# Optimization experiments

Measured on AMD Instinct MI355X. Metric: run time of the kernel, lower is better.

The kernel has to match this reference:

```python
import jax, jax.numpy as jnp
import numpy as np

EPS = 1e-08


def setup_inputs() -> dict:
    key = jax.random.key(0)
    k1, k2 = jax.random.split(key)
    z = jax.random.normal(k1, (32, 768, 32, 32), dtype=jnp.float32)
    memory = jax.random.normal(k2, (512, 768), dtype=jnp.float32)
    return {"z": z, "memory": memory}


def _l2_normalize(x, axis=-1, eps=1e-12):
    # Matches torch F.normalize(dim=-1): x / max(||x||, eps)
    n = jnp.sqrt(jnp.sum(x * x, axis=axis, keepdims=True))
    return x / jnp.maximum(n, eps)


def reference(z, memory):
    B, C, H, W = z.shape
    M = memory.shape[0]
    # (B, C, H, W) -> (B, H*W, C)
    z_flat = jnp.transpose(z, (0, 2, 3, 1)).reshape(B, H * W, C)
    z_norm = _l2_normalize(z_flat)
    mem_norm = _l2_normalize(memory)
    # cosine-similarity scores: (B, N, M)
    scores = jnp.einsum('bnc,mc->bnm', z_norm, mem_norm)
    w = jax.nn.softmax(scores, axis=-1)
    lam = 1.0 / M
    # hard-shrink sparsification: relu(w - lam) * w / (|w - lam| + eps)
    d = w - lam
    attn_w = jax.nn.relu(d) * w / (jnp.abs(d) + EPS)
    attn_w = attn_w / (jnp.sum(attn_w, axis=-1, keepdims=True) + EPS)
    # weighted readout against the RAW (un-normalized) memory
    z_hat_flat = jnp.einsum('bnm,mc->bnc', attn_w, memory)
    z_hat = jnp.transpose(z_hat_flat.reshape(B, H, W, C), (0, 3, 1, 2))
    return (z_hat, attn_w)
```

## Files before the change

### kernel.cpp

```cpp
#include <hip/hip_runtime.h>
#include <hip/hip_bf16.h>
#include <math.h>

typedef short short8 __attribute__((ext_vector_type(8)));
typedef float f32x4 __attribute__((ext_vector_type(4)));
typedef _Float16 f16x8 __attribute__((ext_vector_type(8)));

#define CC 768
#define NN 1024
#define RR 32768
#define MM 512
#define ZSTRIDE 786432
#define OUT_ATTN_OFF 25165824
#define SPLIT_SC 2048.0f
#define INV_SC   (1.0f / 2048.0f)

static __device__ __forceinline__ short f2bf(float f) {
    __hip_bfloat16 h = __float2bfloat16(f);
    return *reinterpret_cast<short*>(&h);
}

static __device__ __forceinline__ double fast_exp_neg(double x) {
    const double LOG2E = 1.4426950408889634074;
    const double LN2   = 0.6931471805599453094;
    const double MAGIC = 6755399441055744.0;
    double t = x * LOG2E;
    double c = t + MAGIC;
    double n = c - MAGIC;
    int ni = (int)__double2loint(c);
    double g = (t - n) * LN2;
    double r = 2.505210838544172e-08;
    r = fma(r, g, 2.755731922398589e-07);
    r = fma(r, g, 2.7557319223985893e-06);
    r = fma(r, g, 2.48015873015873e-05);
    r = fma(r, g, 1.984126984126984e-04);
    r = fma(r, g, 1.388888888888889e-03);
    r = fma(r, g, 8.333333333333333e-03);
    r = fma(r, g, 4.1666666666666664e-02);
    r = fma(r, g, 1.6666666666666666e-01);
    r = fma(r, g, 0.5);
    r = fma(r, g, 1.0);
    r = fma(r, g, 1.0);
    double sc = __hiloint2double((1023 + ni) << 20, 0);
    return r * sc;
}

static __device__ __forceinline__ double fast_rcp(double x) {
    double r = (double)(1.0f / (float)x);
    r = r * (2.0 - x * r);
    r = r * (2.0 - x * r);
    return r;
}

__global__ __launch_bounds__(256) void prep_mem_kernel(const float* __restrict__ memory,
                                                       _Float16* __restrict__ mem_h,
                                                       _Float16* __restrict__ mem_L,
                                                       short* __restrict__ memT_bf) {
    int m = blockIdx.x;
    int t = threadIdx.x;
    double ss = 0.0;
    for (int c = t; c < CC; c += 256) {
        float v = memory[m * CC + c];
        ss += (double)v * (double)v;
    }
    #pragma unroll
    for (int off = 32; off > 0; off >>= 1) ss += __shfl_xor(ss, off);
    __shared__ double red[4];
    __shared__ double invs;
    if ((t & 63) == 0) red[t >> 6] = ss;
    __syncthreads();
    if (t == 0) {
        double tot = red[0] + red[1] + red[2] + red[3];
        invs = 1.0 / fmax(sqrt(tot), 1e-12);
    }
    __syncthreads();
    float inv = (float)invs;
    for (int c = t; c < CC; c += 256) {
        float v  = memory[m * CC + c];
        float nv = v * inv;
        _Float16 h = (_Float16)nv;
        float r1 = nv - (float)h;
        mem_h[m * CC + c] = h;
        mem_L[m * CC + c] = (_Float16)(r1 * SPLIT_SC);
        memT_bf[c * MM + m] = f2bf(v);
    }
}

#define SWZ(row_, k_) ((((row_) << 5) + (k_)) ^ (((row_) & 7) << 3))
__global__ __launch_bounds__(256, 2) void scores_gemm_kernel(const float* __restrict__ z,
                                                             const _Float16* __restrict__ mem_h,
                                                             const _Float16* __restrict__ mem_L,
                                                             float* __restrict__ out_scores,
                                                             double* __restrict__ zinv_ws) {
    __shared__ _Float16 AT[2][2][4096];
    __shared__ _Float16 BT[2][2][4096];
    __shared__ double ssred[256];

    const int t    = threadIdx.x;
    const int lane = t & 63;
    const int wv   = t >> 6;
    const int lrow = lane & 15;
    const int gk   = lane >> 4;
    const int wr   = wv >> 1, wc = wv & 1;
    const int d = blockIdx.x;
    const int colblk = (d >> 3) & 3;
    const int rowblk = (d & 7) | ((d >> 5) << 3);
    const int row0 = rowblk * 128;
    const int b    = row0 >> 10;
    const int n0   = row0 & 1023;
    const int cB0  = colblk * 128;

    const int an   = t & 127;
    const int ak16 = (t >> 7) * 16;
    const float* zA = z + (size_t)b * ZSTRIDE + n0 + an;
    const int bc = t >> 1;
    const int kc = (t & 1) * 16;
    const _Float16* mhB = mem_h + (size_t)(cB0 + bc) * CC + kc;
    const _Float16* mLB = mem_L + (size_t)(cB0 + bc) * CC + kc;

    double ss = 0.0;
    f32x4 am[4][4], ax[4][4];
    #pragma unroll
    for (int fc = 0; fc < 4; ++fc)
        #pragma unroll
        for (int fn = 0; fn < 4; ++fn) {
            am[fc][fn] = (f32x4){0.f, 0.f, 0.f, 0.f};
            ax[fc][fn] = (f32x4){0.f, 0.f, 0.f, 0.f};
        }

    #define LOADS(kt_, av_, bh_, bl_)                                          \
        do {                                                                   \
            _Pragma("unroll")                                                  \
            for (int j = 0; j < 16; ++j)                                       \
                av_[j] = zA[(size_t)((kt_) * 32 + ak16 + j) * NN];             \
            bh_[0] = *reinterpret_cast<const f16x8*>(mhB + (kt_) * 32);        \
            bh_[1] = *reinterpret_cast<const f16x8*>(mhB + (kt_) * 32 + 8);    \
            bl_[0] = *reinterpret_cast<const f16x8*>(mLB + (kt_) * 32);        \
            bl_[1] = *reinterpret_cast<const f16x8*>(mLB + (kt_) * 32 + 8);    \
        } while (0)

    #define WRITES(bb_, av_, bh_, bl_)                                         \
        do {                                                                   \
            f16x8 h8a, l8a, h8b, l8b;                                          \
            _Pragma("unroll")                                                  \
            for (int j = 0; j < 8; ++j) {                                      \
                float v = av_[j];                                              \
                ss = fma((double)v, (double)v, ss);                            \
                _Float16 h = (_Float16)v;                                      \
                h8a[j] = h;                                                    \
                l8a[j] = (_Float16)((v - (float)h) * SPLIT_SC);                \
            }                                                                  \
            _Pragma("unroll")                                                  \
            for (int j = 0; j < 8; ++j) {                                      \
                float v = av_[8 + j];                                          \
                ss = fma((double)v, (double)v, ss);                            \
                _Float16 h = (_Float16)v;                                      \
                h8b[j] = h;                                                    \
                l8b[j] = (_Float16)((v - (float)h) * SPLIT_SC);                \
            }                                                                  \
            *reinterpret_cast<f16x8*>(&AT[bb_][0][SWZ(an, ak16)])     = h8a;   \
            *reinterpret_cast<f16x8*>(&AT[bb_][0][SWZ(an, ak16 + 8)]) = h8b;   \
            *reinterpret_cast<f16x8*>(&AT[bb_][1][SWZ(an, ak16)])     = l8a;   \
            *reinterpret_cast<f16x8*>(&AT[bb_][1][SWZ(an, ak16 + 8)]) = l8b;   \
            *reinterpret_cast<f16x8*>(&BT[bb_][0][SWZ(bc, kc)])       = bh_[0];\
            *reinterpret_cast<f16x8*>(&BT[bb_][0][SWZ(bc, kc + 8)])   = bh_[1];\
            *reinterpret_cast<f16x8*>(&BT[bb_][1][SWZ(bc, kc)])       = bl_[0];\
            *reinterpret_cast<f16x8*>(&BT[bb_][1][SWZ(bc, kc + 8)])   = bl_[1];\
        } while (0)

    {
        float av[16]; f16x8 bh8[2], bl8[2];
        LOADS(0, av, bh8, bl8);
        WRITES(0, av, bh8, bl8);
    }
    __syncthreads();

    #pragma unroll 1
    for (int kt = 0; kt < 24; ++kt) {
        const int cur = kt & 1;
        float av[16]; f16x8 bh8[2], bl8[2];
        if (kt < 23) LOADS(kt + 1, av, bh8, bl8);

        f16x8 ah[4], aL[4];
        #pragma unroll
        for (int fc = 0; fc < 4; ++fc) {
            ah[fc] = *reinterpret_cast<const f16x8*>(&AT[cur][0][SWZ(wr * 64 + fc * 16 + lrow, gk * 8)]);
            aL[fc] = *reinterpret_cast<const f16x8*>(&AT[cur][1][SWZ(wr * 64 + fc * 16 + lrow, gk * 8)]);
        }
        f16x8 bh[4], bL[4];
        #pragma unroll
        for (int fn = 0; fn < 4; ++fn) {
            bh[fn] = *reinterpret_cast<const f16x8*>(&BT[cur][0][SWZ(wc * 64 + fn * 16 + lrow, gk * 8)]);
            bL[fn] = *reinterpret_cast<const f16x8*>(&BT[cur][1][SWZ(wc * 64 + fn * 16 + lrow, gk * 8)]);
        }
        #pragma unroll
        for (int fn = 0; fn < 4; ++fn)
            #pragma unroll
            for (int fc = 0; fc < 4; ++fc) {
                am[fc][fn] = __builtin_amdgcn_mfma_f32_16x16x32_f16(ah[fc], bh[fn], am[fc][fn], 0, 0, 0);
                ax[fc][fn] = __builtin_amdgcn_mfma_f32_16x16x32_f16(aL[fc], bh[fn], ax[fc][fn], 0, 0, 0);
                ax[fc][fn] = __builtin_amdgcn_mfma_f32_16x16x32_f16(ah[fc], bL[fn], ax[fc][fn], 0, 0, 0);
            }

        if (kt < 23) WRITES(cur ^ 1, av, bh8, bl8);
        __syncthreads();
    }
    #undef LOADS
    #undef WRITES

    #pragma unroll
    for (int fc = 0; fc < 4; ++fc)
        #pragma unroll
        for (int fn = 0; fn < 4; ++fn)
            #pragma unroll
            for (int rg = 0; rg < 4; ++rg) {
                int row = row0 + wr * 64 + fc * 16 + gk * 4 + rg;
                int col = cB0 + wc * 64 + fn * 16 + lrow;
                out_scores[(size_t)row * MM + col] = am[fc][fn][rg] + ax[fc][fn][rg] * INV_SC;
            }

    ssred[t] = ss;
    __syncthreads();
    if (colblk == 0 && t < 128) {
        double tot = ssred[t] + ssred[t + 128];
        zinv_ws[row0 + t] = 1.0 / fmax(sqrt(tot), 1e-12);
    }
}
#undef SWZ

__global__ __launch_bounds__(256) void epilogue_kernel(float* __restrict__ attn,
                                                       const double* __restrict__ zinv_ws) {
    const int t    = threadIdx.x;
    const int lane = t & 63;
    const int wv   = t >> 6;
    const int row0 = blockIdx.x * 64;

    #pragma unroll 1
    for (int i = 0; i < 16; ++i) {
        int row = row0 + wv * 16 + i;
        double zi = zinv_ws[row];
        float* rp = attn + (size_t)row * MM;
        f32x4 x0 = *reinterpret_cast<const f32x4*>(&rp[lane * 4]);
        f32x4 x1 = *reinterpret_cast<const f32x4*>(&rp[256 + lane * 4]);
        double s0 = (double)x0[0] * zi, s1 = (double)x0[1] * zi;
        double s2 = (double)x0[2] * zi, s3 = (double)x0[3] * zi;
        double s4 = (double)x1[0] * zi, s5 = (double)x1[1] * zi;
        double s6 = (double)x1[2] * zi, s7 = (double)x1[3] * zi;
        double mx = fmax(fmax(fmax(s0, s1), fmax(s2, s3)),
                         fmax(fmax(s4, s5), fmax(s6, s7)));
        #pragma unroll
        for (int off = 32; off > 0; off >>= 1) mx = fmax(mx, __shfl_xor(mx, off));
        double p0 = fast_exp_neg(s0 - mx), p1 = fast_exp_neg(s1 - mx);
        double p2 = fast_exp_neg(s2 - mx), p3 = fast_exp_neg(s3 - mx);
        double p4 = fast_exp_neg(s4 - mx), p5 = fast_exp_neg(s5 - mx);
        double p6 = fast_exp_neg(s6 - mx), p7 = fast_exp_neg(s7 - mx);
        double Z = ((p0 + p1) + (p2 + p3)) + ((p4 + p5) + (p6 + p7));
        #pragma unroll
        for (int off = 32; off > 0; off >>= 1) Z += __shfl_xor(Z, off);
        double iZ = fast_rcp(Z);
        const double LAM = 1.0 / 512.0;
        double w0 = p0 * iZ, w1 = p1 * iZ, w2 = p2 * iZ, w3 = p3 * iZ;
        double w4 = p4 * iZ, w5 = p5 * iZ, w6 = p6 * iZ, w7 = p7 * iZ;
        double d0 = w0 - LAM, d1 = w1 - LAM, d2 = w2 - LAM, d3 = w3 - LAM;
        double d4 = w4 - LAM, d5 = w5 - LAM, d6 = w6 - LAM, d7 = w7 - LAM;
        double e0 = (d0 > 0.0 ? d0 : 0.0) * w0 * fast_rcp(fabs(d0) + 1e-8);
        double e1 = (d1 > 0.0 ? d1 : 0.0) * w1 * fast_rcp(fabs(d1) + 1e-8);
        double e2 = (d2 > 0.0 ? d2 : 0.0) * w2 * fast_rcp(fabs(d2) + 1e-8);
        double e3 = (d3 > 0.0 ? d3 : 0.0) * w3 * fast_rcp(fabs(d3) + 1e-8);
        double e4 = (d4 > 0.0 ? d4 : 0.0) * w4 * fast_rcp(fabs(d4) + 1e-8);
        double e5 = (d5 > 0.0 ? d5 : 0.0) * w5 * fast_rcp(fabs(d5) + 1e-8);
        double e6 = (d6 > 0.0 ? d6 : 0.0) * w6 * fast_rcp(fabs(d6) + 1e-8);
        double e7 = (d7 > 0.0 ? d7 : 0.0) * w7 * fast_rcp(fabs(d7) + 1e-8);
        double S = ((e0 + e1) + (e2 + e3)) + ((e4 + e5) + (e6 + e7));
        #pragma unroll
        for (int off = 32; off > 0; off >>= 1) S += __shfl_xor(S, off);
        double rinv = fast_rcp(S + 1e-8);
        f32x4 o0 = { (float)(e0 * rinv), (float)(e1 * rinv),
                     (float)(e2 * rinv), (float)(e3 * rinv) };
        f32x4 o1 = { (float)(e4 * rinv), (float)(e5 * rinv),
                     (float)(e6 * rinv), (float)(e7 * rinv) };
        *reinterpret_cast<f32x4*>(&rp[lane * 4])       = o0;
        *reinterpret_cast<f32x4*>(&rp[256 + lane * 4]) = o1;
    }
}

__global__ __launch_bounds__(256, 3) void readout_kernel(const short* __restrict__ memT_bf,
                                                         const float* __restrict__ attn,
                                                         float* __restrict__ out) {
    __shared__ short At[128][40];
    __shared__ short Bt[128][40];
    const int t = threadIdx.x;
    const int d  = blockIdx.x;
    const int xs = d & 7;
    const int hi = d >> 3;
    const int c0idx  = hi % 6;
    const int rowmid = hi / 6;
    const int rb     = xs | (rowmid << 3);
    const int c0     = c0idx * 128;
    const int rowblk = rb * 128;
    const int b  = rowblk >> 10;
    const int nb = rowblk & 1023;
    const int lane = t & 63, wv = t >> 6;
    const int wcr = wv >> 1, wcc = wv & 1;
    const int lrow = lane & 15, gk = lane >> 4;

    f32x4 acc[4][4];
    #pragma unroll
    for (int fc = 0; fc < 4; ++fc)
        #pragma unroll
        for (int fn = 0; fn < 4; ++fn) acc[fc][fn] = (f32x4){0.f, 0.f, 0.f, 0.f};

    const int sr = t >> 1;
    const int ko = (t & 1) * 16;

    for (int m0 = 0; m0 < MM; m0 += 32) {
        __syncthreads();
        {
            const short8* src = reinterpret_cast<const short8*>(
                &memT_bf[(c0 + sr) * MM + m0 + ko]);
            *reinterpret_cast<short8*>(&At[sr][ko])     = src[0];
            *reinterpret_cast<short8*>(&At[sr][ko + 8]) = src[1];
        }
        {
            const f32x4* src = reinterpret_cast<const f32x4*>(
                &attn[(size_t)(rowblk + sr) * MM + m0 + ko]);
            f32x4 v0 = src[0], v1 = src[1], v2 = src[2], v3 = src[3];
            short8 s0 = { f2bf(v0[0]), f2bf(v0[1]), f2bf(v0[2]), f2bf(v0[3]),
                          f2bf(v1[0]), f2bf(v1[1]), f2bf(v1[2]), f2bf(v1[3]) };
            short8 s1 = { f2bf(v2[0]), f2bf(v2[1]), f2bf(v2[2]), f2bf(v2[3]),
                          f2bf(v3[0]), f2bf(v3[1]), f2bf(v3[2]), f2bf(v3[3]) };
            *reinterpret_cast<short8*>(&Bt[sr][ko])     = s0;
            *reinterpret_cast<short8*>(&Bt[sr][ko + 8]) = s1;
        }
        __syncthreads();
        short8 af[4], bf[4];
        #pragma unroll
        for (int fc = 0; fc < 4; ++fc)
            af[fc] = *reinterpret_cast<const short8*>(&At[wcr * 64 + fc * 16 + lrow][gk * 8]);
        #pragma unroll
        for (int fn = 0; fn < 4; ++fn)
            bf[fn] = *reinterpret_cast<const short8*>(&Bt[wcc * 64 + fn * 16 + lrow][gk * 8]);
        #pragma unroll
        for (int fc = 0; fc < 4; ++fc)
            #pragma unroll
            for (int fn = 0; fn < 4; ++fn)
                acc[fc][fn] = __builtin_amdgcn_mfma_f32_16x16x32_bf16(af[fc], bf[fn], acc[fc][fn], 0, 0, 0);
    }

    #pragma unroll
    for (int fc = 0; fc < 4; ++fc)
        #pragma unroll
        for (int fn = 0; fn < 4; ++fn)
            #pragma unroll
            for (int reg = 0; reg < 4; ++reg) {
                int c = c0 + wcr * 64 + fc * 16 + gk * 4 + reg;
                int n = nb + wcc * 64 + fn * 16 + lrow;
                out[(size_t)b * ZSTRIDE + (size_t)c * NN + n] = acc[fc][fn][reg];
            }
}

extern "C" void kernel_launch(void* const* d_in, const int* in_sizes, int n_in,
                              void* d_out, int out_size, void* d_ws, size_t ws_size,
                              hipStream_t stream) {
    const float* z      = (const float*)d_in[0];
    const float* memory = (const float*)d_in[1];
    float* out      = (float*)d_out;
    float* out_attn = out + OUT_ATTN_OFF;

    char* wsb = (char*)d_ws;
    _Float16* mem_h   = (_Float16*)wsb;
    _Float16* mem_L   = (_Float16*)(wsb + 786432);
    short*    memT_bf = (short*)(wsb + 1572864);
    double*   zinv_ws = (double*)(wsb + 2359296);

    prep_mem_kernel<<<512, 256, 0, stream>>>(memory, mem_h, mem_L, memT_bf);
    scores_gemm_kernel<<<1024, 256, 0, stream>>>(z, mem_h, mem_L, out_attn, zinv_ws);
    epilogue_kernel<<<RR / 64, 256, 0, stream>>>(out_attn, zinv_ws);
    readout_kernel<<<1536, 256, 0, stream>>>(memT_bf, out_attn, out);
}
```

Baseline: 197.3 us.

## Use 512-thread blocks in scores GEMM with smaller per-wave tiles and unrolled pipeline

Doubles the scores GEMM block from 256 to 512 threads (8 waves) and halves each wave's row tile, so there are fewer accumulators and fragments per thread. The goal is higher occupancy and better latency hiding. The k-loop is unrolled by two with explicit ping-pong register buffers for the z loads, and s_setprio is raised around the MFMA bursts. The cost is more LDS re-reads of B per block, since each B fragment is reused across fewer rows, plus more barrier participants and register pressure under the 512,4 launch bound.

```diff
diff --git a/kernel.cpp b/kernel.cpp
--- a/kernel.cpp
+++ b/kernel.cpp
@@ -87,14 +87,14 @@
 }
 
 #define SWZ(row_, k_) ((((row_) << 5) + (k_)) ^ (((row_) & 7) << 3))
-__global__ __launch_bounds__(256, 2) void scores_gemm_kernel(const float* __restrict__ z,
+__global__ __launch_bounds__(512, 4) void scores_gemm_kernel(const float* __restrict__ z,
                                                              const _Float16* __restrict__ mem_h,
                                                              const _Float16* __restrict__ mem_L,
                                                              float* __restrict__ out_scores,
                                                              double* __restrict__ zinv_ws) {
     __shared__ _Float16 AT[2][2][4096];
     __shared__ _Float16 BT[2][2][4096];
-    __shared__ double ssred[256];
+    __shared__ double ssred[512];
 
     const int t    = threadIdx.x;
     const int lane = t & 63;
@@ -110,111 +110,121 @@
     const int n0   = row0 & 1023;
     const int cB0  = colblk * 128;
 
-    const int an   = t & 127;
-    const int ak16 = (t >> 7) * 16;
+    const int an  = t & 127;
+    const int ak8 = (t >> 7) * 8;
     const float* zA = z + (size_t)b * ZSTRIDE + n0 + an;
-    const int bc = t >> 1;
-    const int kc = (t & 1) * 16;
+    const int bc = t >> 2;
+    const int kc = (t & 3) * 8;
     const _Float16* mhB = mem_h + (size_t)(cB0 + bc) * CC + kc;
     const _Float16* mLB = mem_L + (size_t)(cB0 + bc) * CC + kc;
 
     double ss = 0.0;
-    f32x4 am[4][4], ax[4][4];
-    #pragma unroll
-    for (int fc = 0; fc < 4; ++fc)
+    f32x4 am[2][4], ax[2][4];
+    #pragma unroll
+    for (int fc = 0; fc < 2; ++fc)
         #pragma unroll
         for (int fn = 0; fn < 4; ++fn) {
             am[fc][fn] = (f32x4){0.f, 0.f, 0.f, 0.f};
             ax[fc][fn] = (f32x4){0.f, 0.f, 0.f, 0.f};
         }
 
-    #define LOADS(kt_, av_, bh_, bl_)                                          \
+    float avX[8], avY[8];
+    f16x8 bh8, bl8;
+
+    #define LOAD_A(kt_, av_)                                                   \
         do {                                                                   \
             _Pragma("unroll")                                                  \
-            for (int j = 0; j < 16; ++j)                                       \
-                av_[j] = zA[(size_t)((kt_) * 32 + ak16 + j) * NN];             \
-            bh_[0] = *reinterpret_cast<const f16x8*>(mhB + (kt_) * 32);        \
-            bh_[1] = *reinterpret_cast<const f16x8*>(mhB + (kt_) * 32 + 8);    \
-            bl_[0] = *reinterpret_cast<const f16x8*>(mLB + (kt_) * 32);        \
-            bl_[1] = *reinterpret_cast<const f16x8*>(mLB + (kt_) * 32 + 8);    \
-        } while (0)
-
-    #define WRITES(bb_, av_, bh_, bl_)                                         \
+            for (int j = 0; j < 8; ++j)                                        \
+                av_[j] = zA[(size_t)((kt_) * 32 + ak8 + j) * NN];              \
+        } while (0)
+
+    #define LOAD_B(kt_)                                                        \
         do {                                                                   \
-            f16x8 h8a, l8a, h8b, l8b;                                          \
+            bh8 = *reinterpret_cast<const f16x8*>(mhB + (kt_) * 32);           \
+            bl8 = *reinterpret_cast<const f16x8*>(mLB + (kt_) * 32);           \
+        } while (0)
+
+    #define WRITE_A(bb_, av_)                                                  \
+        do {                                                                   \
+            f16x8 h8, l8;                                                      \
             _Pragma("unroll")                                                  \
             for (int j = 0; j < 8; ++j) {                                      \
                 float v = av_[j];                                              \
                 ss = fma((double)v, (double)v, ss);                            \
                 _Float16 h = (_Float16)v;                                      \
-                h8a[j] = h;                                                    \
-                l8a[j] = (_Float16)((v - (float)h) * SPLIT_SC);                \
+                h8[j] = h;                                                     \
+                l8[j] = (_Float16)((v - (float)h) * SPLIT_SC);                 \
             }                                                                  \
-            _Pragma("unroll")                                                  \
-            for (int j = 0; j < 8; ++j) {                                      \
-                float v = av_[8 + j];                                          \
-                ss = fma((double)v, (double)v, ss);                            \
-                _Float16 h = (_Float16)v;                                      \
-                h8b[j] = h;                                                    \
-                l8b[j] = (_Float16)((v - (float)h) * SPLIT_SC);                \
-            }                                                                  \
-            *reinterpret_cast<f16x8*>(&AT[bb_][0][SWZ(an, ak16)])     = h8a;   \
-            *reinterpret_cast<f16x8*>(&AT[bb_][0][SWZ(an, ak16 + 8)]) = h8b;   \
-            *reinterpret_cast<f16x8*>(&AT[bb_][1][SWZ(an, ak16)])     = l8a;   \
-            *reinterpret_cast<f16x8*>(&AT[bb_][1][SWZ(an, ak16 + 8)]) = l8b;   \
-            *reinterpret_cast<f16x8*>(&BT[bb_][0][SWZ(bc, kc)])       = bh_[0];\
-            *reinterpret_cast<f16x8*>(&BT[bb_][0][SWZ(bc, kc + 8)])   = bh_[1];\
-            *reinterpret_cast<f16x8*>(&BT[bb_][1][SWZ(bc, kc)])       = bl_[0];\
-            *reinterpret_cast<f16x8*>(&BT[bb_][1][SWZ(bc, kc + 8)])   = bl_[1];\
-        } while (0)
-
-    {
-        float av[16]; f16x8 bh8[2], bl8[2];
-        LOADS(0, av, bh8, bl8);
-        WRITES(0, av, bh8, bl8);
-    }
+            *reinterpret_cast<f16x8*>(&AT[bb_][0][SWZ(an, ak8)]) = h8;         \
+            *reinterpret_cast<f16x8*>(&AT[bb_][1][SWZ(an, ak8)]) = l8;         \
+        } while (0)
+
+    #define WRITE_B(bb_)                                                       \
+        do {                                                                   \
+            *reinterpret_cast<f16x8*>(&BT[bb_][0][SWZ(bc, kc)]) = bh8;         \
+            *reinterpret_cast<f16x8*>(&BT[bb_][1][SWZ(bc, kc)]) = bl8;         \
+        } while (0)
+
+    #define MFMA_BLOCK(cur_)                                                       \
+        do {                                                                       \
+            f16x8 ah0 = *reinterpret_cast<const f16x8*>(                           \
+                &AT[cur_][0][SWZ(wr * 32 + lrow, gk * 8)]);                        \
+            f16x8 ah1 = *reinterpret_cast<const f16x8*>(                           \
+                &AT[cur_][0][SWZ(wr * 32 + 16 + lrow, gk * 8)]);                   \
+            f16x8 aL0 = *reinterpret_cast<const f16x8*>(                           \
+                &AT[cur_][1][SWZ(wr * 32 + lrow, gk * 8)]);                        \
+            f16x8 aL1 = *reinterpret_cast<const f16x8*>(                           \
+                &AT[cur_][1][SWZ(wr * 32 + 16 + lrow, gk * 8)]);                   \
+            __builtin_amdgcn_s_setprio(1);                                         \
+            _Pragma("unroll")                                                      \
+            for (int fn = 0; fn < 4; ++fn) {                                       \
+                f16x8 bhf = *reinterpret_cast<const f16x8*>(                       \
+                    &BT[cur_][0][SWZ(wc * 64 + fn * 16 + lrow, gk * 8)]);          \
+                f16x8 bLf = *reinterpret_cast<const f16x8*>(                       \
+                    &BT[cur_][1][SWZ(wc * 64 + fn * 16 + lrow, gk * 8)]);          \
+                am[0][fn] = __builtin_amdgcn_mfma_f32_16x16x32_f16(ah0, bhf, am[0][fn], 0, 0, 0); \
+                ax[0][fn] = __builtin_amdgcn_mfma_f32_16x16x32_f16(aL0, bhf, ax[0][fn], 0, 0, 0); \
+                ax[0][fn] = __builtin_amdgcn_mfma_f32_16x16x32_f16(ah0, bLf, ax[0][fn], 0, 0, 0); \
+                am[1][fn] = __builtin_amdgcn_mfma_f32_16x16x32_f16(ah1, bhf, am[1][fn], 0, 0, 0); \
+                ax[1][fn] = __builtin_amdgcn_mfma_f32_16x16x32_f16(aL1, bhf, ax[1][fn], 0, 0, 0); \
+                ax[1][fn] = __builtin_amdgcn_mfma_f32_16x16x32_f16(ah1, bLf, ax[1][fn], 0, 0, 0); \
+            }                                                                      \
+            __builtin_amdgcn_s_setprio(0);                                         \
+        } while (0)
+
+    LOAD_A(0, avX);
+    WRITE_A(0, avX);
+    LOAD_B(0);
+    WRITE_B(0);
+    LOAD_A(1, avY);
     __syncthreads();
 
     #pragma unroll 1
-    for (int kt = 0; kt < 24; ++kt) {
-        const int cur = kt & 1;
-        float av[16]; f16x8 bh8[2], bl8[2];
-        if (kt < 23) LOADS(kt + 1, av, bh8, bl8);
-
-        f16x8 ah[4], aL[4];
-        #pragma unroll
-        for (int fc = 0; fc < 4; ++fc) {
-            ah[fc] = *reinterpret_cast<const f16x8*>(&AT[cur][0][SWZ(wr * 64 + fc * 16 + lrow, gk * 8)]);
-            aL[fc] = *reinterpret_cast<const f16x8*>(&AT[cur][1][SWZ(wr * 64 + fc * 16 + lrow, gk * 8)]);
-        }
-        f16x8 bh[4], bL[4];
-        #pragma unroll
-        for (int fn = 0; fn < 4; ++fn) {
-            bh[fn] = *reinterpret_cast<const f16x8*>(&BT[cur][0][SWZ(wc * 64 + fn * 16 + lrow, gk * 8)]);
-            bL[fn] = *reinterpret_cast<const f16x8*>(&BT[cur][1][SWZ(wc * 64 + fn * 16 + lrow, gk * 8)]);
-        }
-        #pragma unroll
-        for (int fn = 0; fn < 4; ++fn)
-            #pragma unroll
-            for (int fc = 0; fc < 4; ++fc) {
-                am[fc][fn] = __builtin_amdgcn_mfma_f32_16x16x32_f16(ah[fc], bh[fn], am[fc][fn], 0, 0, 0);
-                ax[fc][fn] = __builtin_amdgcn_mfma_f32_16x16x32_f16(aL[fc], bh[fn], ax[fc][fn], 0, 0, 0);
-                ax[fc][fn] = __builtin_amdgcn_mfma_f32_16x16x32_f16(ah[fc], bL[fn], ax[fc][fn], 0, 0, 0);
-            }
-
-        if (kt < 23) WRITES(cur ^ 1, av, bh8, bl8);
+    for (int kt = 0; kt < 24; kt += 2) {
+        if (kt + 2 < 24) LOAD_A(kt + 2, avX);
+        if (kt + 1 < 24) LOAD_B(kt + 1);
+        MFMA_BLOCK(0);
+        if (kt + 1 < 24) { WRITE_A(1, avY); WRITE_B(1); }
         __syncthreads();
-    }
-    #undef LOADS
-    #undef WRITES
-
-    #pragma unroll
-    for (int fc = 0; fc < 4; ++fc)
+        if (kt + 3 < 24) LOAD_A(kt + 3, avY);
+        if (kt + 2 < 24) LOAD_B(kt + 2);
+        MFMA_BLOCK(1);
+        if (kt + 2 < 24) { WRITE_A(0, avX); WRITE_B(0); }
+        __syncthreads();
+    }
+    #undef LOAD_A
+    #undef LOAD_B
+    #undef WRITE_A
+    #undef WRITE_B
+    #undef MFMA_BLOCK
+
+    #pragma unroll
+    for (int fc = 0; fc < 2; ++fc)
         #pragma unroll
         for (int fn = 0; fn < 4; ++fn)
             #pragma unroll
             for (int rg = 0; rg < 4; ++rg) {
-                int row = row0 + wr * 64 + fc * 16 + gk * 4 + rg;
+                int row = row0 + wr * 32 + fc * 16 + gk * 4 + rg;
                 int col = cB0 + wc * 64 + fn * 16 + lrow;
                 out_scores[(size_t)row * MM + col] = am[fc][fn][rg] + ax[fc][fn][rg] * INV_SC;
             }
@@ -222,7 +232,7 @@
     ssred[t] = ss;
     __syncthreads();
     if (colblk == 0 && t < 128) {
-        double tot = ssred[t] + ssred[t + 128];
+        double tot = ssred[t] + ssred[t + 128] + ssred[t + 256] + ssred[t + 384];
         zinv_ws[row0 + t] = 1.0 / fmax(sqrt(tot), 1e-12);
     }
 }
@@ -374,7 +384,7 @@
     double*   zinv_ws = (double*)(wsb + 2359296);
 
     prep_mem_kernel<<<512, 256, 0, stream>>>(memory, mem_h, mem_L, memT_bf);
-    scores_gemm_kernel<<<1024, 256, 0, stream>>>(z, mem_h, mem_L, out_attn, zinv_ws);
+    scores_gemm_kernel<<<1024, 512, 0, stream>>>(z, mem_h, mem_L, out_attn, zinv_ws);
     epilogue_kernel<<<RR / 64, 256, 0, stream>>>(out_attn, zinv_ws);
     readout_kernel<<<1536, 256, 0, stream>>>(memT_bf, out_attn, out);
 }
```

New measurement: 312.8 us. 1.59x slower.
